# Kernel optimization log

Measured on AMD Instinct MI355X. Metric: run time of the kernel, lower is better.

The kernel has to match this reference:

```python
import jax, jax.numpy as jnp
import numpy as np

EMBED_DIM = 1024
NUM_HEADS = 16
HEAD_DIM = EMBED_DIM // NUM_HEADS


def setup_inputs() -> dict:
    key = jax.random.key(0)
    k1, k2, k3, k4, k5 = jax.random.split(key, 5)
    B, S, D = 4, 2048, EMBED_DIM
    scale = 1.0 / np.sqrt(D)
    qkv = jax.random.normal(k1, (B, S, D), dtype=jnp.float32)
    W_in = jax.random.uniform(k2, (D, 3 * D), dtype=jnp.float32, minval=-scale, maxval=scale)
    b_in = jax.random.uniform(k3, (3 * D,), dtype=jnp.float32, minval=-scale, maxval=scale)
    W_out = jax.random.uniform(k4, (D, D), dtype=jnp.float32, minval=-scale, maxval=scale)
    b_out = jax.random.uniform(k5, (D,), dtype=jnp.float32, minval=-scale, maxval=scale)
    return {"qkv": qkv, "W_in": W_in, "b_in": b_in, "W_out": W_out, "b_out": b_out}


def reference(qkv, W_in, b_in, W_out, b_out):
    B, S, D = qkv.shape
    H, hd = NUM_HEADS, HEAD_DIM
    proj = qkv @ W_in + b_in                      # [B, S, 3D]
    q, k, v = jnp.split(proj, 3, axis=-1)         # each [B, S, D]
    # reshape to heads: [B, H, S, hd]
    q = q.reshape(B, S, H, hd).transpose(0, 2, 1, 3)
    k = k.reshape(B, S, H, hd).transpose(0, 2, 1, 3)
    v = v.reshape(B, S, H, hd).transpose(0, 2, 1, 3)
    scores = jnp.einsum('bhqd,bhkd->bhqk', q, k) / jnp.sqrt(jnp.float32(hd))
    attn = jax.nn.softmax(scores, axis=-1)        # dropout=0.0 -> identity
    ctx = jnp.einsum('bhqk,bhkd->bhqd', attn, v)  # [B, H, S, hd]
    ctx = ctx.transpose(0, 2, 1, 3).reshape(B, S, D)
    return ctx @ W_out + b_out
```

## Files before the change

kernel.cpp:

```cpp
#include <hip/hip_runtime.h>


typedef __bf16 bf16;
typedef __bf16 bf16x4 __attribute__((ext_vector_type(4)));
typedef __bf16 bf16x8 __attribute__((ext_vector_type(8)));
typedef float f32x4 __attribute__((ext_vector_type(4)));

typedef const __attribute__((address_space(1))) void* gas1p;
typedef __attribute__((address_space(3))) void* las3p;
#define GLD16(g, l) __builtin_amdgcn_global_load_lds((gas1p)(g), (las3p)(l), 16, 0, 0)

#if __has_builtin(__builtin_amdgcn_exp2f)
#define EXP2(x) __builtin_amdgcn_exp2f(x)
#else
#define EXP2(x) exp2f(x)
#endif

__device__ __forceinline__ f32x4 mfma16(bf16x8 a, bf16x8 b, f32x4 c) {
  return __builtin_amdgcn_mfma_f32_16x16x32_bf16(a, b, c, 0, 0, 0);
}

__global__ void prep_kernel(const float* __restrict__ qkv, bf16* __restrict__ Xb,
                            const float* __restrict__ W_in, bf16* __restrict__ WtIn,
                            const float* __restrict__ W_out, bf16* __restrict__ WtOut) {
  __shared__ float tile[32][33];
  int blk = blockIdx.x, tid = threadIdx.x;
  if (blk < 8192) {
    int i = (blk * 256 + tid) * 4;
    float4 v = *(const float4*)(qkv + i);
    bf16x4 o;
    o[0] = (bf16)v.x; o[1] = (bf16)v.y; o[2] = (bf16)v.z; o[3] = (bf16)v.w;
    *(bf16x4*)(Xb + i) = o;
    return;
  }
  const float* in; bf16* out; int R, C, c0, r0;
  if (blk < 11264) {
    int t = blk - 8192; in = W_in; out = WtIn; R = 1024; C = 3072;
    c0 = (t % 96) * 32; r0 = (t / 96) * 32;
  } else {
    int t = blk - 11264; in = W_out; out = WtOut; R = 1024; C = 1024;
    c0 = (t % 32) * 32; r0 = (t / 32) * 32;
  }
  int tx = tid & 31, ty = tid >> 5;
#pragma unroll
  for (int i = 0; i < 4; ++i)
    tile[ty + i * 8][tx] = in[(size_t)(r0 + ty + i * 8) * C + c0 + tx];
  __syncthreads();
#pragma unroll
  for (int i = 0; i < 4; ++i)
    out[(size_t)(c0 + ty + i * 8) * R + r0 + tx] = (bf16)tile[tx][ty + i * 8];
}

__device__ __forceinline__ void stage_tile(const bf16* __restrict__ src, size_t rstride,
                                           int kt, char* dst, int tid) {
#pragma unroll
  for (int i = 0; i < 4; ++i) {
    int chunk = i * 256 + tid;
    int row = chunk >> 3;
    int cs = (chunk & 7) ^ (row & 7);
    GLD16(src + (size_t)row * rstride + kt + cs * 8, dst + chunk * 16);
  }
}

__device__ __forceinline__ void gemm_step(
    const bf16* __restrict__ A, const bf16* __restrict__ B, int m0, int n0,
    const char* ca, const char* cb, char* na, char* nb, int ktn, bool pref,
    int tid, int lane, int quad, int wm, int wn, f32x4 (&acc)[4][4]) {
  if (pref) {
    stage_tile(A + (size_t)m0 * 1024, 1024, ktn, na, tid);
    stage_tile(B + (size_t)n0 * 1024, 1024, ktn, nb, tid);
  }
#pragma unroll
  for (int ks = 0; ks < 2; ++ks) {
    bf16x8 af[4], bfr[4];
#pragma unroll
    for (int t = 0; t < 4; ++t) {
      int ra = wm + t * 16 + (lane & 15);
      af[t] = *(const bf16x8*)(ca + ra * 128 + ((ks * 4 + quad) ^ (ra & 7)) * 16);
      int rb = wn + t * 16 + (lane & 15);
      bfr[t] = *(const bf16x8*)(cb + rb * 128 + ((ks * 4 + quad) ^ (rb & 7)) * 16);
    }
#pragma unroll
    for (int mt = 0; mt < 4; ++mt)
#pragma unroll
      for (int nt = 0; nt < 4; ++nt)
        acc[mt][nt] = mfma16(af[mt], bfr[nt], acc[mt][nt]);
  }
  __syncthreads();
}

__global__ __launch_bounds__(256, 2) void gemm1_kernel(
    const bf16* __restrict__ A, const bf16* __restrict__ Bt, const float* __restrict__ bias,
    bf16* __restrict__ Qo, bf16* __restrict__ Ko, bf16* __restrict__ Vo) {
  __shared__ __align__(16) char sA[2][128 * 64 * 2];
  __shared__ __align__(16) char sB[2][128 * 64 * 2];
  const int tid = threadIdx.x, lane = tid & 63, quad = lane >> 4;
  const int wave = tid >> 6;
  const int id = blockIdx.x, xcd = id & 7, local = id >> 3;
  const int m0 = (xcd * 8 + (local & 7)) * 128, n0 = (local >> 3) * 128;
  const int wm = (wave >> 1) * 64, wn = (wave & 1) * 64;
  f32x4 acc[4][4] = {};

  stage_tile(A + (size_t)m0 * 1024, 1024, 0, sA[0], tid);
  stage_tile(Bt + (size_t)n0 * 1024, 1024, 0, sB[0], tid);
  __syncthreads();
  for (int it = 0; it < 16; it += 2) {
    gemm_step(A, Bt, m0, n0, sA[0], sB[0], sA[1], sB[1], (it + 1) * 64, true,
              tid, lane, quad, wm, wn, acc);
    gemm_step(A, Bt, m0, n0, sA[1], sB[1], sA[0], sB[0], (it + 2) * 64, it + 2 < 16,
              tid, lane, quad, wm, wn, acc);
  }

  const int region = n0 >> 10;
#pragma unroll
  for (int nt = 0; nt < 4; ++nt) {
    int n = n0 + wn + nt * 16 + (lane & 15);
    float bv = bias[n];
    int ncol = n & 1023;
    int h = ncol >> 6, d = ncol & 63;
#pragma unroll
    for (int mt = 0; mt < 4; ++mt) {
      int gm = m0 + wm + mt * 16 + quad * 4;
      int bb = gm >> 11, s = gm & 2047;
      if (region == 2) {
        bf16x4 pk;
#pragma unroll
        for (int r = 0; r < 4; ++r) pk[r] = (bf16)(acc[mt][nt][r] + bv);
        *(bf16x4*)(Vo + ((size_t)((bb * 16 + h) * 64 + d)) * 2048 + s) = pk;
      } else {
        bf16* dst = (region == 0) ? Qo : Ko;
        float scl = (region == 0) ? 0.18033688f : 1.0f;
#pragma unroll
        for (int r = 0; r < 4; ++r)
          dst[((size_t)((bb * 16 + h) * 2048) + s + r) * 64 + d] =
              (bf16)((acc[mt][nt][r] + bv) * scl);
      }
    }
  }
}

__global__ __launch_bounds__(256, 2) void flash_kernel(
    const bf16* __restrict__ Q, const bf16* __restrict__ K, const bf16* __restrict__ Vt,
    bf16* __restrict__ ctx) {
  const int n = blockIdx.x;
  const int bh = (n & 7) * 8 + (n >> 6);
  const int qt = (n >> 3) & 7;
  const int b = bh >> 4, h = bh & 15;
  const int tid = threadIdx.x, lane = tid & 63, wave = tid >> 6, quad = lane >> 4;

  __shared__ __align__(16) char sK[2][128 * 64 * 2];
  __shared__ __align__(16) char sV[2][64 * 128 * 2];
  __shared__ __align__(16) char sP[4][64 * 32 * 2];

  const size_t hb = (size_t)bh * 2048 * 64;
  const int q0 = qt * 256;

#pragma unroll
  for (int i = 0; i < 8; ++i) {
    int chunk = i * 256 + tid;
    int row = chunk >> 3;
    int cs = (chunk & 7) ^ (row & 7);
    char* dst = (i < 4) ? (sK[0] + chunk * 16) : (sK[1] + (chunk - 1024) * 16);
    GLD16(Q + hb + (size_t)(q0 + row) * 64 + cs * 8, dst);
  }
  __syncthreads();
  bf16x8 qf[4][2];
#pragma unroll
  for (int j = 0; j < 4; ++j)
#pragma unroll
    for (int ksd = 0; ksd < 2; ++ksd) {
      int row = wave * 64 + j * 16 + (lane & 15);
      const char* src = sK[row >> 7];
      int r128 = row & 127;
      qf[j][ksd] = *(const bf16x8*)(src + r128 * 128 + ((ksd * 4 + quad) ^ (r128 & 7)) * 16);
    }
  __syncthreads();

#pragma unroll
  for (int i = 0; i < 4; ++i) {
    int chunk = i * 256 + tid;
    int row = chunk >> 3;
    int cs = (chunk & 7) ^ (row & 7);
    GLD16(K + hb + (size_t)row * 64 + cs * 8, sK[0] + chunk * 16);
    int vrow = chunk >> 4;
    int vcs = (chunk & 15) ^ (vrow & 7);
    GLD16(Vt + hb + (size_t)vrow * 2048 + vcs * 8, sV[0] + chunk * 16);
  }
  __syncthreads();

  f32x4 ctxa[4][4] = {};
  float l[4] = {0.f, 0.f, 0.f, 0.f};
  char* pw = sP[wave];

  for (int it = 0; it < 16; ++it) {
    const int kv0 = it * 128;
    if (it < 15) {
      char* nk = sK[(it + 1) & 1];
      char* nv = sV[(it + 1) & 1];
#pragma unroll
      for (int i = 0; i < 4; ++i) {
        int chunk = i * 256 + tid;
        int row = chunk >> 3;
        int cs = (chunk & 7) ^ (row & 7);
        GLD16(K + hb + (size_t)(kv0 + 128 + row) * 64 + cs * 8, nk + chunk * 16);
        int vrow = chunk >> 4;
        int vcs = (chunk & 15) ^ (vrow & 7);
        GLD16(Vt + hb + (size_t)vrow * 2048 + kv0 + 128 + vcs * 8, nv + chunk * 16);
      }
    }
    const char* cb = sK[it & 1];
    const char* vb = sV[it & 1];

#pragma unroll
    for (int kq = 0; kq < 4; ++kq) {
      f32x4 st[2][4] = {};
#pragma unroll
      for (int ksd = 0; ksd < 2; ++ksd) {
        bf16x8 kf[2];
#pragma unroll
        for (int ii = 0; ii < 2; ++ii) {
          int row = kq * 32 + ii * 16 + (lane & 15);
          kf[ii] = *(const bf16x8*)(cb + row * 128 + ((ksd * 4 + quad) ^ (row & 7)) * 16);
        }
#pragma unroll
        for (int ii = 0; ii < 2; ++ii)
#pragma unroll
          for (int j = 0; j < 4; ++j)
            st[ii][j] = mfma16(kf[ii], qf[j][ksd], st[ii][j]);
      }
#pragma unroll
      for (int ii = 0; ii < 2; ++ii)
#pragma unroll
        for (int j = 0; j < 4; ++j) {
          f32x4 p;
#pragma unroll
          for (int r = 0; r < 4; ++r) {
            p[r] = EXP2(st[ii][j][r]);
            l[j] += p[r];
          }
          bf16x4 pk;
#pragma unroll
          for (int r = 0; r < 4; ++r) pk[r] = (bf16)p[r];
          int q = j * 16 + (lane & 15);
          int chunk = ii * 2 + (quad >> 1);
          *(bf16x4*)(pw + q * 64 + ((chunk ^ (q & 3)) * 16) + (quad & 1) * 8) = pk;
        }
      bf16x8 pf[4], vf[4];
#pragma unroll
      for (int mt = 0; mt < 4; ++mt) {
        int q = mt * 16 + (lane & 15);
        pf[mt] = *(const bf16x8*)(pw + q * 64 + ((quad ^ (q & 3)) * 16));
      }
#pragma unroll
      for (int nd = 0; nd < 4; ++nd) {
        int row = nd * 16 + (lane & 15);
        vf[nd] = *(const bf16x8*)(vb + row * 256 + (((kq * 4 + quad) ^ (row & 7)) * 16));
      }
#pragma unroll
      for (int mt = 0; mt < 4; ++mt)
#pragma unroll
        for (int nd = 0; nd < 4; ++nd)
          ctxa[mt][nd] = mfma16(pf[mt], vf[nd], ctxa[mt][nd]);
    }
    __syncthreads();
  }

#pragma unroll
  for (int j = 0; j < 4; ++j) {
    l[j] += __shfl_xor(l[j], 16);
    l[j] += __shfl_xor(l[j], 32);
  }
#pragma unroll
  for (int mt = 0; mt < 4; ++mt)
#pragma unroll
    for (int r = 0; r < 4; ++r) {
      float lsh = __shfl(l[mt], quad * 4 + r);
      float rl = __builtin_amdgcn_rcpf(lsh);
      int srow = q0 + wave * 64 + mt * 16 + quad * 4 + r;
#pragma unroll
      for (int nd = 0; nd < 4; ++nd) {
        int col = h * 64 + nd * 16 + (lane & 15);
        ctx[((size_t)(b * 2048 + srow)) * 1024 + col] = (bf16)(ctxa[mt][nd][r] * rl);
      }
    }
}

__global__ __launch_bounds__(256, 2) void gemm2_kernel(
    const bf16* __restrict__ A, const bf16* __restrict__ Bt, const float* __restrict__ bias,
    float* __restrict__ Out) {
  __shared__ __align__(16) char sA[2][128 * 64 * 2];
  __shared__ __align__(16) char sB[2][128 * 64 * 2];
  const int tid = threadIdx.x, lane = tid & 63, quad = lane >> 4;
  const int wave = tid >> 6;
  const int id = blockIdx.x, xcd = id & 7, local = id >> 3;
  const int m0 = (xcd * 8 + (local & 7)) * 128, n0 = (local >> 3) * 128;
  const int wm = (wave >> 1) * 64, wn = (wave & 1) * 64;
  f32x4 acc[4][4] = {};

  stage_tile(A + (size_t)m0 * 1024, 1024, 0, sA[0], tid);
  stage_tile(Bt + (size_t)n0 * 1024, 1024, 0, sB[0], tid);
  __syncthreads();
  for (int it = 0; it < 16; it += 2) {
    gemm_step(A, Bt, m0, n0, sA[0], sB[0], sA[1], sB[1], (it + 1) * 64, true,
              tid, lane, quad, wm, wn, acc);
    gemm_step(A, Bt, m0, n0, sA[1], sB[1], sA[0], sB[0], (it + 2) * 64, it + 2 < 16,
              tid, lane, quad, wm, wn, acc);
  }

#pragma unroll
  for (int nt = 0; nt < 4; ++nt) {
    int n = n0 + wn + nt * 16 + (lane & 15);
    float bv = bias[n];
#pragma unroll
    for (int mt = 0; mt < 4; ++mt) {
      int gm = m0 + wm + mt * 16 + quad * 4;
#pragma unroll
      for (int r = 0; r < 4; ++r)
        Out[(size_t)(gm + r) * 1024 + n] = acc[mt][nt][r] + bv;
    }
  }
}

extern "C" void kernel_launch(void* const* d_in, const int* in_sizes, int n_in,
                              void* d_out, int out_size, void* d_ws, size_t ws_size,
                              hipStream_t stream) {
  const float* qkv   = (const float*)d_in[0];
  const float* W_in  = (const float*)d_in[1];
  const float* b_in  = (const float*)d_in[2];
  const float* W_out = (const float*)d_in[3];
  const float* b_out = (const float*)d_in[4];
  float* out = (float*)d_out;

  bf16* Xb    = (bf16*)d_ws;
  bf16* WtIn  = Xb + 8388608;
  bf16* WtOut = WtIn + 3145728;
  bf16* Qb    = WtOut + 1048576;
  bf16* Kb    = Qb + 8388608;
  bf16* Vtb   = Kb + 8388608;
  bf16* Ctx   = Xb;

  prep_kernel<<<12288, 256, 0, stream>>>(qkv, Xb, W_in, WtIn, W_out, WtOut);
  gemm1_kernel<<<1536, 256, 0, stream>>>(Xb, WtIn, b_in, Qb, Kb, Vtb);
  flash_kernel<<<512, 256, 0, stream>>>(Qb, Kb, Vtb, Ctx);
  gemm2_kernel<<<512, 256, 0, stream>>>(Ctx, WtOut, b_out, out);
}
```

Baseline: 251.3 us.

## Replace double-buffered GEMM pipeline with single-buffer loop for higher occupancy

Both projection GEMMs drop the LDS double buffer and the prefetch-overlapped step function. They now use a simple loop that syncs, stages one K tile, syncs again and computes. This halves shared memory per block and raises launch bounds from 2 to 4 blocks per CU, so more resident waves can hide load latency in place of explicit software pipelining. The risk is that each block now stalls on every tile load, and occupancy may be capped by the register use of the 64 accumulator floats per thread.

```diff
diff --git a/kernel.cpp b/kernel.cpp
--- a/kernel.cpp
+++ b/kernel.cpp
@@ -62,38 +62,39 @@
   }
 }
 
-__device__ __forceinline__ void gemm_step(
-    const bf16* __restrict__ A, const bf16* __restrict__ B, int m0, int n0,
-    const char* ca, const char* cb, char* na, char* nb, int ktn, bool pref,
-    int tid, int lane, int quad, int wm, int wn, f32x4 (&acc)[4][4]) {
-  if (pref) {
-    stage_tile(A + (size_t)m0 * 1024, 1024, ktn, na, tid);
-    stage_tile(B + (size_t)n0 * 1024, 1024, ktn, nb, tid);
-  }
-#pragma unroll
-  for (int ks = 0; ks < 2; ++ks) {
-    bf16x8 af[4], bfr[4];
-#pragma unroll
-    for (int t = 0; t < 4; ++t) {
-      int ra = wm + t * 16 + (lane & 15);
-      af[t] = *(const bf16x8*)(ca + ra * 128 + ((ks * 4 + quad) ^ (ra & 7)) * 16);
-      int rb = wn + t * 16 + (lane & 15);
-      bfr[t] = *(const bf16x8*)(cb + rb * 128 + ((ks * 4 + quad) ^ (rb & 7)) * 16);
-    }
-#pragma unroll
-    for (int mt = 0; mt < 4; ++mt)
-#pragma unroll
-      for (int nt = 0; nt < 4; ++nt)
-        acc[mt][nt] = mfma16(af[mt], bfr[nt], acc[mt][nt]);
-  }
-  __syncthreads();
-}
-
-__global__ __launch_bounds__(256, 2) void gemm1_kernel(
+__device__ __forceinline__ void gemm_core(
+    const bf16* __restrict__ A, const bf16* __restrict__ Bt, int m0, int n0,
+    char* sA, char* sB, int tid, int lane, int quad, int wm, int wn,
+    f32x4 (&acc)[4][4]) {
+  for (int kt = 0; kt < 1024; kt += 64) {
+    __syncthreads();
+    stage_tile(A + (size_t)m0 * 1024, 1024, kt, sA, tid);
+    stage_tile(Bt + (size_t)n0 * 1024, 1024, kt, sB, tid);
+    __syncthreads();
+#pragma unroll
+    for (int ks = 0; ks < 2; ++ks) {
+      bf16x8 af[4], bfr[4];
+#pragma unroll
+      for (int t = 0; t < 4; ++t) {
+        int ra = wm + t * 16 + (lane & 15);
+        af[t] = *(const bf16x8*)(sA + ra * 128 + ((ks * 4 + quad) ^ (ra & 7)) * 16);
+        int rb = wn + t * 16 + (lane & 15);
+        bfr[t] = *(const bf16x8*)(sB + rb * 128 + ((ks * 4 + quad) ^ (rb & 7)) * 16);
+      }
+#pragma unroll
+      for (int mt = 0; mt < 4; ++mt)
+#pragma unroll
+        for (int nt = 0; nt < 4; ++nt)
+          acc[mt][nt] = mfma16(af[mt], bfr[nt], acc[mt][nt]);
+    }
+  }
+}
+
+__global__ __launch_bounds__(256, 4) void gemm1_kernel(
     const bf16* __restrict__ A, const bf16* __restrict__ Bt, const float* __restrict__ bias,
     bf16* __restrict__ Qo, bf16* __restrict__ Ko, bf16* __restrict__ Vo) {
-  __shared__ __align__(16) char sA[2][128 * 64 * 2];
-  __shared__ __align__(16) char sB[2][128 * 64 * 2];
+  __shared__ __align__(16) char sA[128 * 64 * 2];
+  __shared__ __align__(16) char sB[128 * 64 * 2];
   const int tid = threadIdx.x, lane = tid & 63, quad = lane >> 4;
   const int wave = tid >> 6;
   const int id = blockIdx.x, xcd = id & 7, local = id >> 3;
@@ -101,15 +102,7 @@
   const int wm = (wave >> 1) * 64, wn = (wave & 1) * 64;
   f32x4 acc[4][4] = {};
 
-  stage_tile(A + (size_t)m0 * 1024, 1024, 0, sA[0], tid);
-  stage_tile(Bt + (size_t)n0 * 1024, 1024, 0, sB[0], tid);
-  __syncthreads();
-  for (int it = 0; it < 16; it += 2) {
-    gemm_step(A, Bt, m0, n0, sA[0], sB[0], sA[1], sB[1], (it + 1) * 64, true,
-              tid, lane, quad, wm, wn, acc);
-    gemm_step(A, Bt, m0, n0, sA[1], sB[1], sA[0], sB[0], (it + 2) * 64, it + 2 < 16,
-              tid, lane, quad, wm, wn, acc);
-  }
+  gemm_core(A, Bt, m0, n0, sA, sB, tid, lane, quad, wm, wn, acc);
 
   const int region = n0 >> 10;
 #pragma unroll
@@ -285,11 +278,11 @@
     }
 }
 
-__global__ __launch_bounds__(256, 2) void gemm2_kernel(
+__global__ __launch_bounds__(256, 4) void gemm2_kernel(
     const bf16* __restrict__ A, const bf16* __restrict__ Bt, const float* __restrict__ bias,
     float* __restrict__ Out) {
-  __shared__ __align__(16) char sA[2][128 * 64 * 2];
-  __shared__ __align__(16) char sB[2][128 * 64 * 2];
+  __shared__ __align__(16) char sA[128 * 64 * 2];
+  __shared__ __align__(16) char sB[128 * 64 * 2];
   const int tid = threadIdx.x, lane = tid & 63, quad = lane >> 4;
   const int wave = tid >> 6;
   const int id = blockIdx.x, xcd = id & 7, local = id >> 3;
@@ -297,15 +290,7 @@
   const int wm = (wave >> 1) * 64, wn = (wave & 1) * 64;
   f32x4 acc[4][4] = {};
 
-  stage_tile(A + (size_t)m0 * 1024, 1024, 0, sA[0], tid);
-  stage_tile(Bt + (size_t)n0 * 1024, 1024, 0, sB[0], tid);
-  __syncthreads();
-  for (int it = 0; it < 16; it += 2) {
-    gemm_step(A, Bt, m0, n0, sA[0], sB[0], sA[1], sB[1], (it + 1) * 64, true,
-              tid, lane, quad, wm, wn, acc);
-    gemm_step(A, Bt, m0, n0, sA[1], sB[1], sA[0], sB[0], (it + 2) * 64, it + 2 < 16,
-              tid, lane, quad, wm, wn, acc);
-  }
+  gemm_core(A, Bt, m0, n0, sA, sB, tid, lane, quad, wm, wn, acc);
 
 #pragma unroll
   for (int nt = 0; nt < 4; ++nt) {
```

Measured after the change: 261.0 us. 1.04x slower.
